# Kernel optimization log

Hardware: AMD Instinct MI355X
Metric: run time of the kernel (lower is better)

Reference implementation:

```python
import jax, jax.numpy as jnp
import numpy as np

B, N, C, H = 1024, 49, 1024, 32      # windows, window_area (7*7), dim, heads
HD = C // H                          # 32 head dim
HDL = max(1, int(HD * 0.25))         # 8 lite head dim
LD = HDL * H                         # 256 lite dim
TAB = (2 * 7 - 1) ** 2               # 169 rel-pos table rows
SCALE = HD ** -0.5
SCALE_L = HDL ** -0.5


def setup_inputs() -> dict:
    key = jax.random.key(0)
    ks = jax.random.split(key, 13)
    f = lambda i, shape, s=0.02: jax.random.normal(ks[i], shape, jnp.float32) * s
    return {
        "x": jax.random.normal(ks[0], (B, N, C), jnp.float32),
        "qkv_w": f(1, (C, 3 * C)),           # stored (in, out): y = x @ W + b
        "qkv_b": jnp.zeros((3 * C,), jnp.float32),
        "rpb_table": f(2, (TAB, H)),
        "rel_idx": jax.random.randint(ks[3], (N, N), 0, TAB, dtype=jnp.int32),
        "proj_w": f(4, (C, C)),
        "proj_b": jnp.zeros((C,), jnp.float32),
        "ql_w": f(5, (C, LD)),
        "kl_w": f(6, (C, LD)),
        "vl_w": f(7, (C, LD)),
        "dp_w": f(8, (LD, C), 1e-4),         # diff_proj init std=1e-4
        "dp_b": jnp.zeros((C,), jnp.float32),
        "diff_gamma": jnp.float32(0.02),
        "lam1_raw": jnp.float32(-2.0),
        "lam2_raw": jnp.float32(-2.0),
    }


def _forward(x, qkv_w, qkv_b, rpb_table, proj_w, proj_b,
             ql_w, kl_w, vl_w, dp_w, dp_b,
             diff_gamma, lam1_raw, lam2_raw, rel_idx):
    b, n, c = x.shape
    # qkv projection -> (3, B, H, N, HD)
    qkv = (x @ qkv_w + qkv_b).reshape(b, n, 3, H, HD).transpose(2, 0, 3, 1, 4)
    q, k, v = qkv[0], qkv[1], qkv[2]
    # relative position bias gather -> (1, H, N, N)
    bias = rpb_table[rel_idx.reshape(-1)].reshape(n, n, H).transpose(2, 0, 1)[None]
    attn = jnp.einsum("bhqd,bhkd->bhqk", q * SCALE, k) + bias
    attn_soft = jax.nn.softmax(attn, axis=-1)
    x_out = jnp.einsum("bhqk,bhkd->bhqd", attn_soft, v)
    x_out = x_out.transpose(0, 2, 1, 3).reshape(b, n, c)
    # differential lite branch (dim == 1024 -> use_diff)
    q_l = (x @ ql_w).reshape(b, n, H, HDL).transpose(0, 2, 1, 3)
    k_l = (x @ kl_w).reshape(b, n, H, HDL).transpose(0, 2, 1, 3)
    v_l = (x @ vl_w).reshape(b, n, H, HDL).transpose(0, 2, 1, 3)
    attn_l = jnp.einsum("bhqd,bhkd->bhqk", q_l * SCALE_L, k_l) + bias
    lam1 = jax.nn.sigmoid(lam1_raw)
    lam2 = jax.nn.sigmoid(lam2_raw)
    diff = lam1 * jax.nn.softmax(attn_l, axis=-1) - lam2 * jax.lax.stop_gradient(attn_soft)
    delta_v = jnp.einsum("bhqk,bhkd->bhqd", diff, v_l).transpose(0, 2, 1, 3).reshape(b, n, LD)
    x_out = x_out + diff_gamma * (delta_v @ dp_w + dp_b)
    return x_out @ proj_w + proj_b


def reference(x, qkv_w, qkv_b, rpb_table, rel_idx, proj_w, proj_b,
              ql_w, kl_w, vl_w, dp_w, dp_b, diff_gamma, lam1_raw, lam2_raw):
    return _forward(x, qkv_w, qkv_b, rpb_table, proj_w, proj_b,
                    ql_w, kl_w, vl_w, dp_w, dp_b,
                    diff_gamma, lam1_raw, lam2_raw, rel_idx)
```

## Files before the change

kernel.cpp:

```cpp
#include <hip/hip_runtime.h>
#include <cstdint>
#include <cstddef>

typedef __bf16 bf16_t;
typedef float f32x4 __attribute__((ext_vector_type(4)));
typedef __bf16 bf16x8 __attribute__((ext_vector_type(8)));

#define GLOAD_LDS16(gp, lp)                                                        \
    __builtin_amdgcn_global_load_lds(                                              \
        (const __attribute__((address_space(1))) void*)(gp),                       \
        (__attribute__((address_space(3))) void*)(lp), 16, 0, 0)

template <typename OutT>
__global__ __launch_bounds__(256, 2)
void gemm_bt(const bf16_t* __restrict__ A, const bf16_t* __restrict__ BT,
             OutT* __restrict__ C, const float* __restrict__ bias,
             int M, int K, int ldA, int ldBT, int ldC)
{
    __shared__ __align__(16) bf16_t As[8192];
    __shared__ __align__(16) bf16_t Bs[8192];
    const int bn0 = blockIdx.x * 128;
    const int bm0 = blockIdx.y * 128;
    const int tid  = threadIdx.x;
    const int lane = tid & 63;
    const int w    = tid >> 6;
    const int wr   = w >> 1, wc = w & 1;
    const int lm   = lane & 15, lq = lane >> 4;

    f32x4 acc[4][4];
    #pragma unroll
    for (int i = 0; i < 4; i++)
        #pragma unroll
        for (int j = 0; j < 4; j++) acc[i][j] = (f32x4){0.f, 0.f, 0.f, 0.f};

    const bf16_t* aptr[4];
    const bf16_t* bptr[4];
    #pragma unroll
    for (int ci = 0; ci < 4; ci++) {
        const int c    = w * 4 + ci;
        const int ks   = c >> 3, tile = c & 7;
        const int col  = ks * 32 + lq * 8;
        int arow = bm0 + tile * 16 + lm;
        if (arow > M - 1) arow = M - 1;
        aptr[ci] = A  + (size_t)arow * ldA + col;
        bptr[ci] = BT + (size_t)(bn0 + tile * 16 + lm) * ldBT + col;
    }

    for (int k0 = 0; k0 < K; k0 += 64) {
        __syncthreads();
        #pragma unroll
        for (int ci = 0; ci < 4; ci++) {
            const int c = w * 4 + ci;
            GLOAD_LDS16(aptr[ci] + k0, &As[c * 512]);
            GLOAD_LDS16(bptr[ci] + k0, &Bs[c * 512]);
        }
        __syncthreads();
        #pragma unroll
        for (int ks = 0; ks < 2; ks++) {
            bf16x8 af[4], bfr[4];
            #pragma unroll
            for (int t = 0; t < 4; t++) {
                af[t]  = *(const bf16x8*)&As[(ks * 8 + wr * 4 + t) * 512 + lane * 8];
                bfr[t] = *(const bf16x8*)&Bs[(ks * 8 + wc * 4 + t) * 512 + lane * 8];
            }
            #pragma unroll
            for (int mt = 0; mt < 4; mt++)
                #pragma unroll
                for (int nt = 0; nt < 4; nt++)
                    acc[mt][nt] = __builtin_amdgcn_mfma_f32_16x16x32_bf16(
                        af[mt], bfr[nt], acc[mt][nt], 0, 0, 0);
        }
    }

    float bv[4];
    #pragma unroll
    for (int nt = 0; nt < 4; nt++)
        bv[nt] = bias ? bias[bn0 + wc * 64 + nt * 16 + lm] : 0.f;
    #pragma unroll
    for (int mt = 0; mt < 4; mt++)
        #pragma unroll
        for (int r = 0; r < 4; r++) {
            const int row = bm0 + wr * 64 + mt * 16 + lq * 4 + r;
            if (row >= M) continue;
            OutT* cp = C + (size_t)row * ldC + bn0 + wc * 64 + lm;
            #pragma unroll
            for (int nt = 0; nt < 4; nt++)
                cp[nt * 16] = (OutT)(acc[mt][nt][r] + bv[nt]);
        }
}

template <typename SrcT>
__global__ void transpose_to_bf16(const SrcT* __restrict__ src, bf16_t* __restrict__ dst,
                                  int K, int N, int ldsrc, int lddst,
                                  const float* __restrict__ scale_ptr)
{
    __shared__ float tile[32][33];
    const int k0 = blockIdx.x * 32, n0 = blockIdx.y * 32;
    const int tx = threadIdx.x & 31, ty = threadIdx.x >> 5;
    #pragma unroll
    for (int i = 0; i < 4; i++) {
        int k = k0 + ty + 8 * i;
        tile[ty + 8 * i][tx] = (k < K && n0 + tx < N)
            ? (float)src[(size_t)k * ldsrc + n0 + tx] : 0.f;
    }
    __syncthreads();
    const float s = scale_ptr ? *scale_ptr : 1.0f;
    #pragma unroll
    for (int i = 0; i < 4; i++) {
        int n = n0 + ty + 8 * i, k = k0 + tx;
        if (n < N && k < K)
            dst[(size_t)n * lddst + k] = (bf16_t)(s * tile[tx][ty + 8 * i]);
    }
}

__global__ void cast_f32_bf16(const float* __restrict__ src, bf16_t* __restrict__ dst, long n)
{
    long i = ((long)blockIdx.x * blockDim.x + threadIdx.x) * 4;
    if (i >= n) return;
    const float4 v = *(const float4*)(src + i);
    bf16_t d0 = (bf16_t)v.x, d1 = (bf16_t)v.y, d2 = (bf16_t)v.z, d3 = (bf16_t)v.w;
    dst[i] = d0; dst[i + 1] = d1; dst[i + 2] = d2; dst[i + 3] = d3;
}

__global__ void prep_biasA(const float* __restrict__ qkv_b, float* __restrict__ biasA) {
    int n = blockIdx.x * 256 + threadIdx.x;
    if (n < 3840) biasA[n] = (n < 3072) ? qkv_b[n] : 0.f;
}

__global__ void prep_biasO(const float* __restrict__ proj_b, const float* __restrict__ dp_b,
                           const float* __restrict__ proj_w, const float* __restrict__ dgamma,
                           float* __restrict__ biasO) {
    int n = blockIdx.x * 256 + threadIdx.x;
    if (n >= 1024) return;
    float acc = 0.f;
    for (int m = 0; m < 1024; m++) acc += dp_b[m] * proj_w[m * 1024 + n];
    biasO[n] = proj_b[n] + (*dgamma) * acc;
}

__global__ void prep_biasH(const float* __restrict__ rpb, const int* __restrict__ rel,
                           float* __restrict__ biasH) {
    int t = blockIdx.x * 256 + threadIdx.x;
    if (t >= 32 * 49 * 49) return;
    int h = t & 31, ij = t >> 5;
    biasH[(size_t)h * 2401 + ij] = rpb[(size_t)rel[ij] * 32 + h];
}

__global__ __launch_bounds__(64)
void attn_kernel(const bf16_t* __restrict__ QKVL, const float* __restrict__ biasH,
                 bf16_t* __restrict__ AD,
                 const float* __restrict__ lam1p, const float* __restrict__ lam2p)
{
    constexpr float SCALE   = 0.17677669529663687f;
    constexpr float SCALE_L = 0.35355339059327373f;
    const int h  = blockIdx.x & 31;
    const int wb = blockIdx.x >> 5;
    const int lane = threadIdx.x;
    __shared__ float Ks[49][32];
    __shared__ float Vs[49][32];
    __shared__ float KLs[49][8];
    __shared__ float VLs[49][8];
    const size_t base = (size_t)wb * 49 * 3840;

    for (int idx = lane; idx < 196; idx += 64) {
        const int r = idx >> 2, s = idx & 3;
        const bf16x8 kv = *(const bf16x8*)(QKVL + base + (size_t)r * 3840 + 1024 + h * 32 + s * 8);
        const bf16x8 vv = *(const bf16x8*)(QKVL + base + (size_t)r * 3840 + 2048 + h * 32 + s * 8);
        #pragma unroll
        for (int e = 0; e < 8; e++) { Ks[r][s * 8 + e] = (float)kv[e]; Vs[r][s * 8 + e] = (float)vv[e]; }
    }
    for (int r = lane; r < 49; r += 64) {
        const bf16x8 kl = *(const bf16x8*)(QKVL + base + (size_t)r * 3840 + 3328 + h * 8);
        const bf16x8 vl = *(const bf16x8*)(QKVL + base + (size_t)r * 3840 + 3584 + h * 8);
        #pragma unroll
        for (int e = 0; e < 8; e++) { KLs[r][e] = (float)kl[e]; VLs[r][e] = (float)vl[e]; }
    }
    __syncthreads();
    const int i = lane;
    if (i >= 49) return;

    float q[32], qlv[8];
    const bf16_t* qp = QKVL + base + (size_t)i * 3840 + h * 32;
    #pragma unroll
    for (int s = 0; s < 4; s++) {
        const bf16x8 t = *(const bf16x8*)(qp + s * 8);
        #pragma unroll
        for (int e = 0; e < 8; e++) q[s * 8 + e] = (float)t[e] * SCALE;
    }
    {
        const bf16x8 t = *(const bf16x8*)(QKVL + base + (size_t)i * 3840 + 3072 + h * 8);
        #pragma unroll
        for (int e = 0; e < 8; e++) qlv[e] = (float)t[e] * SCALE_L;
    }
    const float* bias = biasH + ((size_t)h * 49 + i) * 49;

    float lg[49], lgl[49];
    #pragma unroll
    for (int j = 0; j < 49; j++) {
        float d = 0.f;
        #pragma unroll
        for (int dd = 0; dd < 32; dd++) d += q[dd] * Ks[j][dd];
        lg[j] = d + bias[j];
    }
    #pragma unroll
    for (int j = 0; j < 49; j++) {
        float d = 0.f;
        #pragma unroll
        for (int dd = 0; dd < 8; dd++) d += qlv[dd] * KLs[j][dd];
        lgl[j] = d + bias[j];
    }
    float m1 = -1e30f, m2 = -1e30f;
    #pragma unroll
    for (int j = 0; j < 49; j++) { m1 = fmaxf(m1, lg[j]); m2 = fmaxf(m2, lgl[j]); }
    float s1 = 0.f, s2 = 0.f;
    #pragma unroll
    for (int j = 0; j < 49; j++) {
        lg[j]  = __expf(lg[j]  - m1); s1 += lg[j];
        lgl[j] = __expf(lgl[j] - m2); s2 += lgl[j];
    }
    const float r1 = 1.f / s1, r2 = 1.f / s2;
    const float l1 = 1.f / (1.f + __expf(-*lam1p));
    const float l2 = 1.f / (1.f + __expf(-*lam2p));

    float o[32], ov[8];
    #pragma unroll
    for (int dd = 0; dd < 32; dd++) o[dd] = 0.f;
    #pragma unroll
    for (int dd = 0; dd < 8; dd++) ov[dd] = 0.f;
    #pragma unroll
    for (int j = 0; j < 49; j++) {
        const float a  = lg[j] * r1;
        const float df = l1 * (lgl[j] * r2) - l2 * a;
        #pragma unroll
        for (int dd = 0; dd < 32; dd++) o[dd] += a * Vs[j][dd];
        #pragma unroll
        for (int dd = 0; dd < 8; dd++)  ov[dd] += df * VLs[j][dd];
    }
    bf16_t* orow = AD + ((size_t)wb * 49 + i) * 1280;
    #pragma unroll
    for (int s = 0; s < 4; s++) {
        bf16x8 t;
        #pragma unroll
        for (int e = 0; e < 8; e++) t[e] = (bf16_t)o[s * 8 + e];
        *(bf16x8*)(orow + h * 32 + s * 8) = t;
    }
    {
        bf16x8 t;
        #pragma unroll
        for (int e = 0; e < 8; e++) t[e] = (bf16_t)ov[e];
        *(bf16x8*)(orow + 1024 + h * 8) = t;
    }
}

extern "C" void kernel_launch(void* const* d_in, const int* in_sizes, int n_in,
                              void* d_out, int out_size, void* d_ws, size_t ws_size,
                              hipStream_t stream)
{
    const float* x      = (const float*)d_in[0];
    const float* qkv_w  = (const float*)d_in[1];
    const float* qkv_b  = (const float*)d_in[2];
    const float* rpb    = (const float*)d_in[3];
    const int*   rel    = (const int*)d_in[4];
    const float* proj_w = (const float*)d_in[5];
    const float* proj_b = (const float*)d_in[6];
    const float* ql_w   = (const float*)d_in[7];
    const float* kl_w   = (const float*)d_in[8];
    const float* vl_w   = (const float*)d_in[9];
    const float* dp_w   = (const float*)d_in[10];
    const float* dp_b   = (const float*)d_in[11];
    const float* dgamma = (const float*)d_in[12];
    const float* lam1   = (const float*)d_in[13];
    const float* lam2   = (const float*)d_in[14];
    float* out = (float*)d_out;
    (void)in_sizes; (void)n_in; (void)out_size;

    char* p = (char*)d_ws;
    auto alloc = [&](size_t bytes) { char* r = p; p += (bytes + 255) & ~(size_t)255; return r; };
    bf16_t* W1T   = (bf16_t*)alloc((size_t)3840 * 1024 * 2);
    bf16_t* W2T   = (bf16_t*)alloc((size_t)1024 * 1280 * 2);
    bf16_t* DPb   = (bf16_t*)alloc((size_t)256 * 1024 * 2);
    bf16_t* Ptmp  = (bf16_t*)alloc((size_t)256 * 1024 * 2);
    float*  biasA = (float*) alloc(3840 * 4);
    float*  biasO = (float*) alloc(1024 * 4);
    float*  biasH = (float*) alloc((size_t)32 * 2401 * 4);
    const size_t fixed = (size_t)(p - (char*)d_ws);
    int CB = 1024;
    while (CB > 1 && fixed + (size_t)CB * 49 * 6144 * 2 + 1024 > ws_size) CB >>= 1;
    bf16_t* Xb   = (bf16_t*)alloc((size_t)CB * 49 * 1024 * 2);
    bf16_t* QKVL = (bf16_t*)alloc((size_t)CB * 49 * 3840 * 2);
    bf16_t* AD   = (bf16_t*)alloc((size_t)CB * 49 * 1280 * 2);

    transpose_to_bf16<float><<<dim3(32, 96), 256, 0, stream>>>(qkv_w, W1T,                     1024, 3072, 3072, 1024, nullptr);
    transpose_to_bf16<float><<<dim3(32, 8),  256, 0, stream>>>(ql_w,  W1T + (size_t)3072*1024, 1024, 256,  256,  1024, nullptr);
    transpose_to_bf16<float><<<dim3(32, 8),  256, 0, stream>>>(kl_w,  W1T + (size_t)3328*1024, 1024, 256,  256,  1024, nullptr);
    transpose_to_bf16<float><<<dim3(32, 8),  256, 0, stream>>>(vl_w,  W1T + (size_t)3584*1024, 1024, 256,  256,  1024, nullptr);
    transpose_to_bf16<float><<<dim3(32, 32), 256, 0, stream>>>(proj_w, W2T,                    1024, 1024, 1024, 1280, nullptr);
    cast_f32_bf16<<<dim3((256 * 1024 / 4 + 255) / 256), 256, 0, stream>>>(dp_w, DPb, 256 * 1024);
    gemm_bt<bf16_t><<<dim3(8, 2), 256, 0, stream>>>(DPb, W2T, Ptmp, nullptr, 256, 1024, 1024, 1280, 1024);
    transpose_to_bf16<bf16_t><<<dim3(8, 32), 256, 0, stream>>>(Ptmp, W2T + 1024, 256, 1024, 1024, 1280, dgamma);
    prep_biasA<<<dim3(15), 256, 0, stream>>>(qkv_b, biasA);
    prep_biasO<<<dim3(4),  256, 0, stream>>>(proj_b, dp_b, proj_w, dgamma, biasO);
    prep_biasH<<<dim3((32 * 2401 + 255) / 256), 256, 0, stream>>>(rpb, rel, biasH);

    const int nchunk = 1024 / CB;
    const int Mc = CB * 49;
    const int gy = (Mc + 127) / 128;
    for (int cc = 0; cc < nchunk; cc++) {
        const float* xc = x + (size_t)cc * Mc * 1024;
        cast_f32_bf16<<<dim3(((long)Mc * 1024 / 4 + 255) / 256), 256, 0, stream>>>(xc, Xb, (long)Mc * 1024);
        gemm_bt<bf16_t><<<dim3(3840 / 128, gy), 256, 0, stream>>>(
            Xb, W1T, QKVL, biasA, Mc, 1024, 1024, 1024, 3840);
        attn_kernel<<<dim3(CB * 32), 64, 0, stream>>>(QKVL, biasH, AD, lam1, lam2);
        gemm_bt<float><<<dim3(1024 / 128, gy), 256, 0, stream>>>(
            AD, W2T, out + (size_t)cc * Mc * 1024, biasO, Mc, 1280, 1280, 1280, 1024);
    }
}
```

Before: 1.863 ms.

## Double-buffer LDS tiles in bf16 GEMM to overlap loads with MFMA

The GEMM kernel now keeps two LDS buffers for the A and B tiles and issues the global-to-LDS loads for the next K step before computing on the current one. This removes one of the two barriers per iteration and is meant to hide global load latency behind the MFMA work. LDS use doubles to 64 KB per block, which can lower occupancy against the launch_bounds target of 2 blocks per CU. The single barrier relies on the async global_load_lds being complete by the barrier, with no explicit vmcnt wait, so correctness depends on how the compiler places waits.

```diff
diff --git a/kernel.cpp b/kernel.cpp
--- a/kernel.cpp
+++ b/kernel.cpp
@@ -17,8 +17,9 @@
              OutT* __restrict__ C, const float* __restrict__ bias,
              int M, int K, int ldA, int ldBT, int ldC)
 {
-    __shared__ __align__(16) bf16_t As[8192];
-    __shared__ __align__(16) bf16_t Bs[8192];
+    __shared__ __align__(16) bf16_t As[2][8192];
+    __shared__ __align__(16) bf16_t Bs[2][8192];
+
     const int bn0 = blockIdx.x * 128;
     const int bm0 = blockIdx.y * 128;
     const int tid  = threadIdx.x;
@@ -46,46 +47,59 @@
         bptr[ci] = BT + (size_t)(bn0 + tile * 16 + lm) * ldBT + col;
     }
 
-    for (int k0 = 0; k0 < K; k0 += 64) {
-        __syncthreads();
-        #pragma unroll
-        for (int ci = 0; ci < 4; ci++) {
-            const int c = w * 4 + ci;
-            GLOAD_LDS16(aptr[ci] + k0, &As[c * 512]);
-            GLOAD_LDS16(bptr[ci] + k0, &Bs[c * 512]);
+    const int nt = K >> 6;
+
+    #pragma unroll
+    for (int ci = 0; ci < 4; ci++) {
+        const int c = w * 4 + ci;
+        GLOAD_LDS16(aptr[ci], &As[0][c * 512]);
+        GLOAD_LDS16(bptr[ci], &Bs[0][c * 512]);
+    }
+    __syncthreads();
+
+    for (int t = 0; t < nt; ++t) {
+        const int cur = t & 1;
+        if (t + 1 < nt) {
+            const int k0 = (t + 1) << 6;
+            #pragma unroll
+            for (int ci = 0; ci < 4; ci++) {
+                const int c = w * 4 + ci;
+                GLOAD_LDS16(aptr[ci] + k0, &As[cur ^ 1][c * 512]);
+                GLOAD_LDS16(bptr[ci] + k0, &Bs[cur ^ 1][c * 512]);
+            }
         }
-        __syncthreads();
         #pragma unroll
         for (int ks = 0; ks < 2; ks++) {
             bf16x8 af[4], bfr[4];
             #pragma unroll
-            for (int t = 0; t < 4; t++) {
-                af[t]  = *(const bf16x8*)&As[(ks * 8 + wr * 4 + t) * 512 + lane * 8];
-                bfr[t] = *(const bf16x8*)&Bs[(ks * 8 + wc * 4 + t) * 512 + lane * 8];
+            for (int t4 = 0; t4 < 4; t4++) {
+                af[t4]  = *(const bf16x8*)&As[cur][(ks * 8 + wr * 4 + t4) * 512 + lane * 8];
+                bfr[t4] = *(const bf16x8*)&Bs[cur][(ks * 8 + wc * 4 + t4) * 512 + lane * 8];
             }
             #pragma unroll
             for (int mt = 0; mt < 4; mt++)
                 #pragma unroll
-                for (int nt = 0; nt < 4; nt++)
-                    acc[mt][nt] = __builtin_amdgcn_mfma_f32_16x16x32_bf16(
-                        af[mt], bfr[nt], acc[mt][nt], 0, 0, 0);
+                for (int nt2 = 0; nt2 < 4; nt2++)
+                    acc[mt][nt2] = __builtin_amdgcn_mfma_f32_16x16x32_bf16(
+                        af[mt], bfr[nt2], acc[mt][nt2], 0, 0, 0);
         }
+        __syncthreads();
     }
 
     float bv[4];
     #pragma unroll
-    for (int nt = 0; nt < 4; nt++)
-        bv[nt] = bias ? bias[bn0 + wc * 64 + nt * 16 + lm] : 0.f;
+    for (int nt2 = 0; nt2 < 4; nt2++)
+        bv[nt2] = bias ? bias[bn0 + wc * 64 + nt2 * 16 + lm] : 0.f;
     #pragma unroll
     for (int mt = 0; mt < 4; mt++)
         #pragma unroll
-        for (int r = 0; r < 4; r++) {
-            const int row = bm0 + wr * 64 + mt * 16 + lq * 4 + r;
+        for (int r2 = 0; r2 < 4; r2++) {
+            const int row = bm0 + wr * 64 + mt * 16 + lq * 4 + r2;
             if (row >= M) continue;
             OutT* cp = C + (size_t)row * ldC + bn0 + wc * 64 + lm;
             #pragma unroll
-            for (int nt = 0; nt < 4; nt++)
-                cp[nt * 16] = (OutT)(acc[mt][nt][r] + bv[nt]);
+            for (int nt2 = 0; nt2 < 4; nt2++)
+                cp[nt2 * 16] = (OutT)(acc[mt][nt2][r2] + bv[nt2]);
         }
 }
 
```

Result: slower. 2.018 ms (+8.3%).
